# Kernel optimization log

Measured on AMD Instinct MI355X. Metric: run time of the kernel, lower is better.

Reference implementation:

```python
import jax, jax.numpy as jnp
import numpy as np

N = 100000
E = 1600000
IN_C, HID, OUT_C = 128, 64, 64


def gcn_conv(x, src, dst, W, b, n):
    # PyG GCNConv: h = D^{-1/2} (A + I) D^{-1/2} (x @ W) + b
    h = x @ W  # [N, F_out]
    # degrees from edges + self-loops (edge weight 1)
    deg = jax.ops.segment_sum(jnp.ones_like(dst, dtype=h.dtype), dst, num_segments=n)
    deg = deg + 1.0  # self-loops
    dinv = jnp.where(deg > 0, jax.lax.rsqrt(deg), 0.0)
    norm = dinv[src] * dinv[dst]  # [E]
    out = jax.ops.segment_sum(h[src] * norm[:, None], dst, num_segments=n)
    out = out + h * (dinv * dinv)[:, None]  # self-loop messages
    return out + b


def setup_inputs() -> dict:
    key = jax.random.key(0)
    ks = jax.random.split(key, 8)
    x = jax.random.normal(ks[0], (N, IN_C), dtype=jnp.float32)
    edge_index = jax.random.randint(ks[1], (2, E), 0, N, dtype=jnp.int64)
    def glorot(k, fan_in, fan_out):
        s = jnp.sqrt(6.0 / (fan_in + fan_out))
        return jax.random.uniform(k, (fan_in, fan_out), jnp.float32, -s, s)
    return {
        "x": x,
        "edge_index": edge_index,
        "W1": glorot(ks[2], IN_C, HID),
        "b1": jnp.zeros((HID,), jnp.float32),
        "W_mu": glorot(ks[3], HID, OUT_C),
        "b_mu": jnp.zeros((OUT_C,), jnp.float32),
        "W_ls": glorot(ks[4], HID, OUT_C),
        "b_ls": jnp.zeros((OUT_C,), jnp.float32),
    }


def reference(x, edge_index, W1, b1, W_mu, b_mu, W_ls, b_ls):
    src, dst = edge_index[0], edge_index[1]
    h = jax.nn.relu(gcn_conv(x, src, dst, W1, b1, N))
    mu = gcn_conv(h, src, dst, W_mu, b_mu, N)
    logstd = gcn_conv(h, src, dst, W_ls, b_ls, N)
    return mu, logstd
```

## Files before the change

kernel.cpp:

```cpp
#include <hip/hip_runtime.h>


using uint = unsigned int;

static constexpr int FEAT = 64;
static constexpr int BN = 256;
static constexpr int SORT_BLOCKS = 256;
static constexpr int SORT_TPB = 1024;
static constexpr int NB_MAX = 512;
static constexpr int AGG_TPB = 1024;
static constexpr int ECAP = 5120;

typedef __attribute__((ext_vector_type(8))) short bf16x8;
typedef __attribute__((ext_vector_type(4))) float f32x4;

static __device__ __forceinline__ ushort f2bf(float f) {
    uint u = __float_as_uint(f);
    u += 0x7FFFu + ((u >> 16) & 1u);
    return (ushort)(u >> 16);
}
static __device__ __forceinline__ float bf2f(ushort b) {
    return __uint_as_float(((uint)b) << 16);
}


__global__ __launch_bounds__(SORT_TPB) void hist_kernel(const int* __restrict__ dst,
                                                        int* __restrict__ hist, int E, int nb) {
    __shared__ int h[NB_MAX];
    for (int i = threadIdx.x; i < nb; i += SORT_TPB) h[i] = 0;
    __syncthreads();
    int chunk = (E + SORT_BLOCKS - 1) / SORT_BLOCKS;
    int beg = blockIdx.x * chunk;
    int end = min(beg + chunk, E);
    for (int e = beg + (int)threadIdx.x; e < end; e += SORT_TPB)
        atomicAdd(&h[dst[e] >> 8], 1);
    __syncthreads();
    for (int i = threadIdx.x; i < nb; i += SORT_TPB) hist[blockIdx.x * nb + i] = h[i];
}

__global__ __launch_bounds__(256) void colscan_kernel(int* __restrict__ hist,
                                                      int* __restrict__ btot, int nb) {
    __shared__ int s[256];
    int b = blockIdx.x;
    int t = threadIdx.x;
    int v = hist[t * nb + b];
    s[t] = v; __syncthreads();
    for (int off = 1; off < 256; off <<= 1) {
        int u = (t >= off) ? s[t - off] : 0;
        __syncthreads();
        s[t] += u;
        __syncthreads();
    }
    hist[t * nb + b] = s[t] - v;
    if (t == 255) btot[b] = s[255];
}

__global__ __launch_bounds__(256) void bbase_kernel(const int* __restrict__ btot,
                                                    int* __restrict__ bbase, int nb) {
    __shared__ int s[256];
    int t = threadIdx.x;
    int i0 = 2 * t, i1 = 2 * t + 1;
    int v0 = (i0 < nb) ? btot[i0] : 0;
    int v1 = (i1 < nb) ? btot[i1] : 0;
    s[t] = v0 + v1; __syncthreads();
    for (int off = 1; off < 256; off <<= 1) {
        int u = (t >= off) ? s[t - off] : 0;
        __syncthreads();
        s[t] += u;
        __syncthreads();
    }
    int excl = s[t] - (v0 + v1);
    if (i0 <= nb) bbase[i0] = excl;
    if (i1 <= nb) bbase[i1] = excl + v0;
}

__global__ __launch_bounds__(SORT_TPB) void sort_scatter_kernel(const int* __restrict__ src,
                                                                const int* __restrict__ dst,
                                                                const int* __restrict__ hist,
                                                                const int* __restrict__ bbase,
                                                                uint* __restrict__ bpk,
                                                                int E, int nb) {
    __shared__ int cur[NB_MAX];
    int k = blockIdx.x;
    for (int i = threadIdx.x; i < nb; i += SORT_TPB) cur[i] = bbase[i] + hist[k * nb + i];
    __syncthreads();
    int chunk = (E + SORT_BLOCKS - 1) / SORT_BLOCKS;
    int beg = k * chunk;
    int end = min(beg + chunk, E);
    for (int e = beg + (int)threadIdx.x; e < end; e += SORT_TPB) {
        int s = src[e], d = dst[e];
        int pos = atomicAdd(&cur[d >> 8], 1);
        bpk[pos] = (uint)s | ((uint)(d & 255) << 17);
    }
}

__global__ __launch_bounds__(SORT_TPB) void dinv_bpk_kernel(const uint* __restrict__ bpk,
                                                            const int* __restrict__ bbase,
                                                            float* __restrict__ dinv, int n) {
    __shared__ int cnt[BN];
    int b = blockIdx.x;
    int base = b * BN;
    int t = threadIdx.x;
    int beg = bbase[b], end = bbase[b + 1];
    if (t < BN) cnt[t] = 0;
    __syncthreads();
    for (int p = beg + t; p < end; p += SORT_TPB)
        atomicAdd(&cnt[(bpk[p] >> 17) & 255], 1);
    __syncthreads();
    int node = base + t;
    if (t < BN && node < n) dinv[node] = rsqrtf((float)cnt[t] + 1.0f);
}

__global__ __launch_bounds__(256) void prep_w_kernel(const float* __restrict__ W1,
                                                     const float* __restrict__ Wmu,
                                                     const float* __restrict__ Wls,
                                                     ushort* __restrict__ w1t,
                                                     ushort* __restrict__ wmt,
                                                     ushort* __restrict__ wlt) {
    int t = blockIdx.x * 256 + threadIdx.x;
    for (int idx = t; idx < 64 * 128; idx += 2048) {
        int nn = idx >> 7, kk = idx & 127;
        w1t[idx] = f2bf(W1[kk * 64 + nn]);
    }
    for (int idx = t; idx < 64 * 64; idx += 2048) {
        int nn = idx >> 6, kk = idx & 63;
        wmt[idx] = f2bf(Wmu[kk * 64 + nn]);
        wlt[idx] = f2bf(Wls[kk * 64 + nn]);
    }
}

__global__ __launch_bounds__(256) void gemm1_kernel(const float* __restrict__ X,
                                                    const ushort* __restrict__ Wt,
                                                    const float* __restrict__ dinv,
                                                    ushort* __restrict__ T1, int n) {
    int lane = threadIdx.x & 63;
    int w = threadIdx.x >> 6;
    int rowbase = blockIdx.x * 64 + w * 16;
    int nl = lane & 15;
    int kg = lane >> 4;
    int arow = min(rowbase + nl, n - 1);
    const float* xr = X + (size_t)arow * 128 + kg * 8;
    f32x4 acc0 = {0.f, 0.f, 0.f, 0.f};
    f32x4 acc1 = acc0, acc2 = acc0, acc3 = acc0;
#pragma unroll
    for (int ks = 0; ks < 4; ++ks) {
        int k0 = ks * 32;
        float4 xa = *(const float4*)(xr + k0);
        float4 xb = *(const float4*)(xr + k0 + 4);
        bf16x8 a;
        a[0] = (short)f2bf(xa.x); a[1] = (short)f2bf(xa.y);
        a[2] = (short)f2bf(xa.z); a[3] = (short)f2bf(xa.w);
        a[4] = (short)f2bf(xb.x); a[5] = (short)f2bf(xb.y);
        a[6] = (short)f2bf(xb.z); a[7] = (short)f2bf(xb.w);
        const ushort* wb = Wt + (size_t)nl * 128 + k0 + kg * 8;
        bf16x8 b0 = *(const bf16x8*)(wb);
        bf16x8 b1 = *(const bf16x8*)(wb + 16 * 128);
        bf16x8 b2 = *(const bf16x8*)(wb + 32 * 128);
        bf16x8 b3 = *(const bf16x8*)(wb + 48 * 128);
        acc0 = __builtin_amdgcn_mfma_f32_16x16x32_bf16(a, b0, acc0, 0, 0, 0);
        acc1 = __builtin_amdgcn_mfma_f32_16x16x32_bf16(a, b1, acc1, 0, 0, 0);
        acc2 = __builtin_amdgcn_mfma_f32_16x16x32_bf16(a, b2, acc2, 0, 0, 0);
        acc3 = __builtin_amdgcn_mfma_f32_16x16x32_bf16(a, b3, acc3, 0, 0, 0);
    }
#pragma unroll
    for (int r = 0; r < 4; ++r) {
        int row = rowbase + kg * 4 + r;
        if (row < n) {
            float di = dinv[row];
            ushort* out = T1 + (size_t)row * FEAT + nl;
            out[0]  = f2bf(acc0[r] * di);
            out[16] = f2bf(acc1[r] * di);
            out[32] = f2bf(acc2[r] * di);
            out[48] = f2bf(acc3[r] * di);
        }
    }
}

template<int MODE>
__global__ __launch_bounds__(AGG_TPB) void agg_kernel(const ushort* __restrict__ T,
                                                      const uint* __restrict__ bpk,
                                                      const int* __restrict__ bbase,
                                                      const float* __restrict__ bias,
                                                      ushort* __restrict__ Tout, int n) {
    __shared__ int lsrc[ECAP];
    __shared__ int cnt[BN];
    __shared__ int cur[BN];
    __shared__ int sc[BN];
    int b = blockIdx.x;
    int base = b * BN;
    int t = threadIdx.x;
    int beg = bbase[b], end = bbase[b + 1];
    if (t < BN) cnt[t] = 0;
    __syncthreads();
    for (int p = beg + t; p < end; p += AGG_TPB)
        atomicAdd(&cnt[(bpk[p] >> 17) & 255], 1);
    __syncthreads();
    if (t < BN) sc[t] = cnt[t];
    __syncthreads();
    for (int off = 1; off < BN; off <<= 1) {
        int u = 0;
        if (t < BN && t >= off) u = sc[t - off];
        __syncthreads();
        if (t < BN) sc[t] += u;
        __syncthreads();
    }
    if (t < BN) cur[t] = sc[t] - cnt[t];
    __syncthreads();
    for (int p = beg + t; p < end; p += AGG_TPB) {
        uint e = bpk[p];
        int pos = atomicAdd(&cur[(e >> 17) & 255], 1);
        lsrc[pos] = (int)(e & 0x1FFFFu);
    }
    __syncthreads();
    int f = t & 63;
    int w = t >> 6;
    for (int nl = w; nl < BN; nl += 16) {
        int node = base + nl;
        if (node >= n) break;
        int c = cnt[nl];
        int pe = sc[nl];
        int p = pe - c;
        float acc = bf2f(T[(size_t)node * FEAT + f]);
        for (; p + 8 <= pe; p += 8) {
            int s0 = lsrc[p],     s1 = lsrc[p + 1], s2 = lsrc[p + 2], s3 = lsrc[p + 3];
            int s4 = lsrc[p + 4], s5 = lsrc[p + 5], s6 = lsrc[p + 6], s7 = lsrc[p + 7];
            float v0 = bf2f(T[(size_t)s0 * FEAT + f]);
            float v1 = bf2f(T[(size_t)s1 * FEAT + f]);
            float v2 = bf2f(T[(size_t)s2 * FEAT + f]);
            float v3 = bf2f(T[(size_t)s3 * FEAT + f]);
            float v4 = bf2f(T[(size_t)s4 * FEAT + f]);
            float v5 = bf2f(T[(size_t)s5 * FEAT + f]);
            float v6 = bf2f(T[(size_t)s6 * FEAT + f]);
            float v7 = bf2f(T[(size_t)s7 * FEAT + f]);
            acc += ((v0 + v1) + (v2 + v3)) + ((v4 + v5) + (v6 + v7));
        }
        for (; p < pe; ++p) acc += bf2f(T[(size_t)lsrc[p] * FEAT + f]);
        float di = rsqrtf((float)c + 1.0f);
        if (MODE == 0) {
            float h = fmaf(di, acc, bias[f]);
            h = fmaxf(h, 0.0f);
            Tout[(size_t)node * FEAT + f] = f2bf(h * di);
        } else {
            Tout[(size_t)node * FEAT + f] = f2bf(di * acc);
        }
    }
}

__global__ __launch_bounds__(256) void gemm_dual_kernel(const ushort* __restrict__ H,
                                                        const ushort* __restrict__ Wmt,
                                                        const float* __restrict__ bmu,
                                                        const ushort* __restrict__ Wlt,
                                                        const float* __restrict__ bls,
                                                        float* __restrict__ mu,
                                                        float* __restrict__ ls, int n) {
    int lane = threadIdx.x & 63;
    int w = threadIdx.x >> 6;
    int rowbase = blockIdx.x * 64 + w * 16;
    int nl = lane & 15;
    int kg = lane >> 4;
    int arow = min(rowbase + nl, n - 1);
    const ushort* hr = H + (size_t)arow * 64 + kg * 8;
    f32x4 am0 = {0.f, 0.f, 0.f, 0.f};
    f32x4 am1 = am0, am2 = am0, am3 = am0;
    f32x4 al0 = am0, al1 = am0, al2 = am0, al3 = am0;
#pragma unroll
    for (int ks = 0; ks < 2; ++ks) {
        int k0 = ks * 32;
        bf16x8 a = *(const bf16x8*)(hr + k0);
        const ushort* wm = Wmt + (size_t)nl * 64 + k0 + kg * 8;
        const ushort* wl = Wlt + (size_t)nl * 64 + k0 + kg * 8;
        bf16x8 m0 = *(const bf16x8*)(wm);
        bf16x8 m1 = *(const bf16x8*)(wm + 16 * 64);
        bf16x8 m2 = *(const bf16x8*)(wm + 32 * 64);
        bf16x8 m3 = *(const bf16x8*)(wm + 48 * 64);
        bf16x8 l0 = *(const bf16x8*)(wl);
        bf16x8 l1 = *(const bf16x8*)(wl + 16 * 64);
        bf16x8 l2 = *(const bf16x8*)(wl + 32 * 64);
        bf16x8 l3 = *(const bf16x8*)(wl + 48 * 64);
        am0 = __builtin_amdgcn_mfma_f32_16x16x32_bf16(a, m0, am0, 0, 0, 0);
        am1 = __builtin_amdgcn_mfma_f32_16x16x32_bf16(a, m1, am1, 0, 0, 0);
        am2 = __builtin_amdgcn_mfma_f32_16x16x32_bf16(a, m2, am2, 0, 0, 0);
        am3 = __builtin_amdgcn_mfma_f32_16x16x32_bf16(a, m3, am3, 0, 0, 0);
        al0 = __builtin_amdgcn_mfma_f32_16x16x32_bf16(a, l0, al0, 0, 0, 0);
        al1 = __builtin_amdgcn_mfma_f32_16x16x32_bf16(a, l1, al1, 0, 0, 0);
        al2 = __builtin_amdgcn_mfma_f32_16x16x32_bf16(a, l2, al2, 0, 0, 0);
        al3 = __builtin_amdgcn_mfma_f32_16x16x32_bf16(a, l3, al3, 0, 0, 0);
    }
    float bm0 = bmu[nl], bm1 = bmu[16 + nl], bm2 = bmu[32 + nl], bm3 = bmu[48 + nl];
    float bl0 = bls[nl], bl1 = bls[16 + nl], bl2 = bls[32 + nl], bl3 = bls[48 + nl];
#pragma unroll
    for (int r = 0; r < 4; ++r) {
        int row = rowbase + kg * 4 + r;
        if (row < n) {
            float* om = mu + (size_t)row * 64 + nl;
            float* ol = ls + (size_t)row * 64 + nl;
            om[0]  = am0[r] + bm0; om[16] = am1[r] + bm1;
            om[32] = am2[r] + bm2; om[48] = am3[r] + bm3;
            ol[0]  = al0[r] + bl0; ol[16] = al1[r] + bl1;
            ol[32] = al2[r] + bl2; ol[48] = al3[r] + bl3;
        }
    }
}

extern "C" void kernel_launch(void* const* d_in, const int* in_sizes, int n_in,
                              void* d_out, int out_size, void* d_ws, size_t ws_size,
                              hipStream_t stream) {
    const float* x   = (const float*)d_in[0];
    const int*   ei  = (const int*)d_in[1];
    const float* W1  = (const float*)d_in[2];
    const float* b1  = (const float*)d_in[3];
    const float* Wmu = (const float*)d_in[4];
    const float* bmu = (const float*)d_in[5];
    const float* Wls = (const float*)d_in[6];
    const float* bls = (const float*)d_in[7];

    const int N = in_sizes[0] / 128;
    const int E = in_sizes[1] / 2;
    const int* src = ei;
    const int* dst = ei + E;

    const int nb = (N + BN - 1) / BN;

    float*  dinv   = (float*)d_ws;
    int*    hist   = (int*)(dinv + N);
    int*    btot   = hist + SORT_BLOCKS * nb;
    int*    bbase  = btot + ((nb + 63) & ~63);
    uint*   bpk    = (uint*)(bbase + ((nb + 1 + 63) & ~63));
    ushort* T1     = (ushort*)(bpk + E);
    ushort* T2     = T1 + (size_t)N * FEAT;
    ushort* w1t    = T2 + (size_t)N * FEAT;
    ushort* wmt    = w1t + 64 * 128;
    ushort* wlt    = wmt + 64 * 64;

    float* mu_out = (float*)d_out;
    float* ls_out = mu_out + (size_t)N * FEAT;

    const int TB = 256;
    int grid_g = (N + 63) / 64;

    prep_w_kernel<<<8, TB, 0, stream>>>(W1, Wmu, Wls, w1t, wmt, wlt);

    hist_kernel<<<SORT_BLOCKS, SORT_TPB, 0, stream>>>(dst, hist, E, nb);
    colscan_kernel<<<nb, TB, 0, stream>>>(hist, btot, nb);
    bbase_kernel<<<1, TB, 0, stream>>>(btot, bbase, nb);
    sort_scatter_kernel<<<SORT_BLOCKS, SORT_TPB, 0, stream>>>(src, dst, hist, bbase, bpk, E, nb);
    dinv_bpk_kernel<<<nb, SORT_TPB, 0, stream>>>(bpk, bbase, dinv, N);

    gemm1_kernel<<<grid_g, TB, 0, stream>>>(x, w1t, dinv, T1, N);

    agg_kernel<0><<<nb, AGG_TPB, 0, stream>>>(T1, bpk, bbase, b1, T2, N);

    agg_kernel<1><<<nb, AGG_TPB, 0, stream>>>(T2, bpk, bbase, nullptr, T1, N);

    gemm_dual_kernel<<<grid_g, TB, 0, stream>>>(T1, wmt, bmu, wlt, bls, mu_out, ls_out, N);
}
```

Before: 187.8 us.

## Fuse weight prep into histogram kernel and merge column/block scans

Folds the weight transpose/bf16 conversion into an extra block of the histogram kernel. It also merges the per-bucket column scan and the global bucket-base scan into one kernel, which uses wave shuffle scans and a last-block-done atomic counter. Together these remove two kernel launches and the serial dependencies between them. The cost is a counter in workspace, reset by the hist kernel, and a threadfence-based last-block pattern. The final scan assumes nb is at most 448 (64 lanes times 7).

```diff
diff --git a/kernel.cpp b/kernel.cpp
--- a/kernel.cpp
+++ b/kernel.cpp
@@ -23,9 +23,30 @@
     return __uint_as_float(((uint)b) << 16);
 }
 
-
 __global__ __launch_bounds__(SORT_TPB) void hist_kernel(const int* __restrict__ dst,
-                                                        int* __restrict__ hist, int E, int nb) {
+                                                        int* __restrict__ hist,
+                                                        const float* __restrict__ W1,
+                                                        const float* __restrict__ Wmu,
+                                                        const float* __restrict__ Wls,
+                                                        ushort* __restrict__ w1t,
+                                                        ushort* __restrict__ wmt,
+                                                        ushort* __restrict__ wlt,
+                                                        int* __restrict__ done,
+                                                        int E, int nb) {
+    if (blockIdx.x == SORT_BLOCKS) {
+        int t = threadIdx.x;
+        if (t == 0) *done = 0;
+        for (int idx = t; idx < 64 * 128; idx += SORT_TPB) {
+            int nn = idx >> 7, kk = idx & 127;
+            w1t[idx] = f2bf(W1[kk * 64 + nn]);
+        }
+        for (int idx = t; idx < 64 * 64; idx += SORT_TPB) {
+            int nn = idx >> 6, kk = idx & 63;
+            wmt[idx] = f2bf(Wmu[kk * 64 + nn]);
+            wlt[idx] = f2bf(Wls[kk * 64 + nn]);
+        }
+        return;
+    }
     __shared__ int h[NB_MAX];
     for (int i = threadIdx.x; i < nb; i += SORT_TPB) h[i] = 0;
     __syncthreads();
@@ -38,40 +59,60 @@
     for (int i = threadIdx.x; i < nb; i += SORT_TPB) hist[blockIdx.x * nb + i] = h[i];
 }
 
-__global__ __launch_bounds__(256) void colscan_kernel(int* __restrict__ hist,
-                                                      int* __restrict__ btot, int nb) {
-    __shared__ int s[256];
-    int b = blockIdx.x;
-    int t = threadIdx.x;
-    int v = hist[t * nb + b];
-    s[t] = v; __syncthreads();
-    for (int off = 1; off < 256; off <<= 1) {
-        int u = (t >= off) ? s[t - off] : 0;
-        __syncthreads();
-        s[t] += u;
-        __syncthreads();
-    }
-    hist[t * nb + b] = s[t] - v;
-    if (t == 255) btot[b] = s[255];
-}
-
-__global__ __launch_bounds__(256) void bbase_kernel(const int* __restrict__ btot,
-                                                    int* __restrict__ bbase, int nb) {
-    __shared__ int s[256];
-    int t = threadIdx.x;
-    int i0 = 2 * t, i1 = 2 * t + 1;
-    int v0 = (i0 < nb) ? btot[i0] : 0;
-    int v1 = (i1 < nb) ? btot[i1] : 0;
-    s[t] = v0 + v1; __syncthreads();
-    for (int off = 1; off < 256; off <<= 1) {
-        int u = (t >= off) ? s[t - off] : 0;
-        __syncthreads();
-        s[t] += u;
-        __syncthreads();
-    }
-    int excl = s[t] - (v0 + v1);
-    if (i0 <= nb) bbase[i0] = excl;
-    if (i1 <= nb) bbase[i1] = excl + v0;
+__global__ __launch_bounds__(1024) void colscan_kernel(int* __restrict__ hist,
+                                                       int* __restrict__ btot,
+                                                       int* __restrict__ bbase,
+                                                       int* __restrict__ done, int nb) {
+    __shared__ int lastflag;
+    int wave = threadIdx.x >> 6;
+    int lane = threadIdx.x & 63;
+    int b = blockIdx.x * 16 + wave;
+    if (b < nb) {
+        int v[4]; int lsum = 0;
+#pragma unroll
+        for (int j = 0; j < 4; ++j) { v[j] = hist[(4 * lane + j) * nb + b]; lsum += v[j]; }
+        int incl = lsum;
+#pragma unroll
+        for (int off = 1; off < 64; off <<= 1) {
+            int t = __shfl_up(incl, off, 64);
+            if (lane >= off) incl += t;
+        }
+        int e = incl - lsum;
+#pragma unroll
+        for (int j = 0; j < 4; ++j) { hist[(4 * lane + j) * nb + b] = e; e += v[j]; }
+        if (lane == 63) btot[b] = incl;
+    }
+    __syncthreads();
+    if (threadIdx.x == 0) {
+        __threadfence();
+        int prev = atomicAdd(done, 1);
+        lastflag = (prev == (int)gridDim.x - 1) ? 1 : 0;
+    }
+    __syncthreads();
+    if (lastflag && wave == 0) {
+        __threadfence();
+        int v[7]; int lsum = 0;
+        int base = lane * 7;
+#pragma unroll
+        for (int j = 0; j < 7; ++j) {
+            int i = base + j;
+            int x = (i < nb) ? btot[i] : 0;
+            v[j] = x; lsum += x;
+        }
+        int incl = lsum;
+#pragma unroll
+        for (int off = 1; off < 64; off <<= 1) {
+            int t = __shfl_up(incl, off, 64);
+            if (lane >= off) incl += t;
+        }
+        int e = incl - lsum;
+#pragma unroll
+        for (int j = 0; j < 7; ++j) {
+            int i = base + j;
+            if (i <= nb) bbase[i] = e;
+            e += v[j];
+        }
+    }
 }
 
 __global__ __launch_bounds__(SORT_TPB) void sort_scatter_kernel(const int* __restrict__ src,
@@ -109,24 +150,6 @@
     __syncthreads();
     int node = base + t;
     if (t < BN && node < n) dinv[node] = rsqrtf((float)cnt[t] + 1.0f);
-}
-
-__global__ __launch_bounds__(256) void prep_w_kernel(const float* __restrict__ W1,
-                                                     const float* __restrict__ Wmu,
-                                                     const float* __restrict__ Wls,
-                                                     ushort* __restrict__ w1t,
-                                                     ushort* __restrict__ wmt,
-                                                     ushort* __restrict__ wlt) {
-    int t = blockIdx.x * 256 + threadIdx.x;
-    for (int idx = t; idx < 64 * 128; idx += 2048) {
-        int nn = idx >> 7, kk = idx & 127;
-        w1t[idx] = f2bf(W1[kk * 64 + nn]);
-    }
-    for (int idx = t; idx < 64 * 64; idx += 2048) {
-        int nn = idx >> 6, kk = idx & 63;
-        wmt[idx] = f2bf(Wmu[kk * 64 + nn]);
-        wlt[idx] = f2bf(Wls[kk * 64 + nn]);
-    }
 }
 
 __global__ __launch_bounds__(256) void gemm1_kernel(const float* __restrict__ X,
@@ -214,6 +237,7 @@
     __syncthreads();
     int f = t & 63;
     int w = t >> 6;
+    float bias_f = (MODE == 0) ? bias[f] : 0.0f;
     for (int nl = w; nl < BN; nl += 16) {
         int node = base + nl;
         if (node >= n) break;
@@ -237,7 +261,7 @@
         for (; p < pe; ++p) acc += bf2f(T[(size_t)lsrc[p] * FEAT + f]);
         float di = rsqrtf((float)c + 1.0f);
         if (MODE == 0) {
-            float h = fmaf(di, acc, bias[f]);
+            float h = fmaf(di, acc, bias_f);
             h = fmaxf(h, 0.0f);
             Tout[(size_t)node * FEAT + f] = f2bf(h * di);
         } else {
@@ -325,7 +349,8 @@
     int*    hist   = (int*)(dinv + N);
     int*    btot   = hist + SORT_BLOCKS * nb;
     int*    bbase  = btot + ((nb + 63) & ~63);
-    uint*   bpk    = (uint*)(bbase + ((nb + 1 + 63) & ~63));
+    int*    done   = bbase + ((nb + 1 + 63) & ~63);
+    uint*   bpk    = (uint*)(done + 64);
     ushort* T1     = (ushort*)(bpk + E);
     ushort* T2     = T1 + (size_t)N * FEAT;
     ushort* w1t    = T2 + (size_t)N * FEAT;
@@ -337,12 +362,11 @@
 
     const int TB = 256;
     int grid_g = (N + 63) / 64;
-
-    prep_w_kernel<<<8, TB, 0, stream>>>(W1, Wmu, Wls, w1t, wmt, wlt);
-
-    hist_kernel<<<SORT_BLOCKS, SORT_TPB, 0, stream>>>(dst, hist, E, nb);
-    colscan_kernel<<<nb, TB, 0, stream>>>(hist, btot, nb);
-    bbase_kernel<<<1, TB, 0, stream>>>(btot, bbase, nb);
+    int grid_cs = (nb + 15) / 16;
+
+    hist_kernel<<<SORT_BLOCKS + 1, SORT_TPB, 0, stream>>>(dst, hist, W1, Wmu, Wls,
+                                                          w1t, wmt, wlt, done, E, nb);
+    colscan_kernel<<<grid_cs, 1024, 0, stream>>>(hist, btot, bbase, done, nb);
     sort_scatter_kernel<<<SORT_BLOCKS, SORT_TPB, 0, stream>>>(src, dst, hist, bbase, bpk, E, nb);
     dinv_bpk_kernel<<<nb, SORT_TPB, 0, stream>>>(bpk, bbase, dinv, N);
 
```

Measured after the change: 189.9 us. No clear change (+1.1%).
